# Optimization experiments

Hardware: AMD Instinct MI355X
Metric: run time of the kernel (lower is better)

## Reference

```python
import jax, jax.numpy as jnp
import numpy as np

N_NODES = 50000
N_EDGES = 800000
IN_CH = 128
OUT_CH = 32
HID = 2 * OUT_CH  # 64


def setup_inputs() -> dict:
    key = jax.random.key(0)
    ks = jax.random.split(key, 8)
    x = jax.random.normal(ks[0], (N_NODES, IN_CH), dtype=jnp.float32)
    edge_index = jax.random.randint(ks[1], (2, N_EDGES), 0, N_NODES, dtype=jnp.int32)
    s1 = 1.0 / np.sqrt(IN_CH)
    s2 = 1.0 / np.sqrt(HID)
    W1 = jax.random.normal(ks[2], (IN_CH, HID), dtype=jnp.float32) * s1
    b1 = jnp.zeros((HID,), dtype=jnp.float32)
    W_mu = jax.random.normal(ks[3], (HID, OUT_CH), dtype=jnp.float32) * s2
    b_mu = jnp.zeros((OUT_CH,), dtype=jnp.float32)
    W_logstd = jax.random.normal(ks[4], (HID, OUT_CH), dtype=jnp.float32) * s2
    b_logstd = jnp.zeros((OUT_CH,), dtype=jnp.float32)
    return {"x": x, "edge_index": edge_index, "W1": W1, "b1": b1,
            "W_mu": W_mu, "b_mu": b_mu, "W_logstd": W_logstd, "b_logstd": b_logstd}


def _gcn_norm(edge_index, n, dtype):
    # PyG GCNConv: add self-loops, symmetric normalization D^-1/2 A D^-1/2
    loops = jnp.arange(n, dtype=edge_index.dtype)
    src = jnp.concatenate([edge_index[0], loops])
    dst = jnp.concatenate([edge_index[1], loops])
    deg = jax.ops.segment_sum(jnp.ones_like(dst, dtype=dtype), dst, num_segments=n)
    deg_inv_sqrt = jnp.where(deg > 0, jax.lax.rsqrt(deg), 0.0)
    norm = deg_inv_sqrt[src] * deg_inv_sqrt[dst]  # [E+N]
    return src, dst, norm


def _gcn_conv(x, W, b, src, dst, norm, n):
    h = x @ W                        # transform first (in >= out)
    msg = h[src] * norm[:, None]     # gather + scale, [E+N, out]
    out = jax.ops.segment_sum(msg, dst, num_segments=n)
    return out + b


def reference(x, edge_index, W1, b1, W_mu, b_mu, W_logstd, b_logstd):
    n = x.shape[0]
    src, dst, norm = _gcn_norm(edge_index, n, x.dtype)
    h = jax.nn.relu(_gcn_conv(x, W1, b1, src, dst, norm, n))
    mu = _gcn_conv(h, W_mu, b_mu, src, dst, norm, n)
    logstd = _gcn_conv(h, W_logstd, b_logstd, src, dst, norm, n)
    return mu, logstd
```

## Files before the change

### kernel.cpp

```cpp
#include <hip/hip_runtime.h>
#include <hip/hip_fp16.h>

#define N_NODES 50000
#define N_EDGES 800000
#define IN_CH 128
#define HID 64
#define OUT_CH 32
#define CAP 64
#define ZROW N_NODES
#define CURS 16

union H4 { uint2 u; __half2 h[2]; };

__global__ __launch_bounds__(256) void k_scatter(const int* __restrict__ ei,
                                                 int* cur, unsigned short* __restrict__ pk,
                                                 unsigned* zA, unsigned* zB) {
    if (blockIdx.x == 0 && threadIdx.x < 32) { zA[threadIdx.x] = 0u; zB[threadIdx.x] = 0u; }
    int g = blockIdx.x * 256 + threadIdx.x;
    if (g >= N_EDGES / 2) return;
    int2 ss = ((const int2*)ei)[g];
    int2 dd = ((const int2*)(ei + N_EDGES))[g];
    int p0 = (dd.x << 6) + atomicAdd(&cur[dd.x << 4], 1);
    pk[p0] = (unsigned short)ss.x;
    int p1 = (dd.y << 6) + atomicAdd(&cur[dd.y << 4], 1);
    pk[p1] = (unsigned short)ss.y;
}

__global__ __launch_bounds__(256) void k_mm1(const float* __restrict__ x,
                                             const float* __restrict__ W1,
                                             const int* __restrict__ cur,
                                             __half* __restrict__ t1) {
    __shared__ float4 ws[64 * 16];
    __shared__ float  xsT[64 * 64];
    int t = threadIdx.x;
    int n0 = blockIdx.x * 64;
    int lane = t & 63, wv_ = t >> 6;
    int ni = lane >> 2;
    int cq = ((lane & 3) << 2) + wv_;
    const float4* W4 = (const float4*)W1;
    const float4* x4 = (const float4*)x;
    float4 acc0 = {0,0,0,0}, acc1 = acc0, acc2 = acc0, acc3 = acc0;
#pragma unroll
    for (int kt = 0; kt < 2; ++kt) {
        __syncthreads();
#pragma unroll
        for (int i = 0; i < 4; ++i) {
            int L = i * 256 + t;
            ws[L] = W4[kt * 1024 + L];
            int n = L >> 4, q = L & 15;
            int ng = n0 + n; if (ng >= N_NODES) ng = N_NODES - 1;
            float4 v = x4[ng * 32 + kt * 16 + q];
            int fb = q * 256 + (((n >> 2) ^ q) << 2) + (n & 3);
            xsT[fb]       = v.x;
            xsT[fb + 64]  = v.y;
            xsT[fb + 128] = v.z;
            xsT[fb + 192] = v.w;
        }
        __syncthreads();
        const float4* xsT4 = (const float4*)xsT;
#pragma unroll 8
        for (int k = 0; k < 64; ++k) {
            float4 xv = xsT4[k * 16 + (ni ^ (k >> 2))];
            float4 wvv = ws[k * 16 + cq];
            acc0.x += xv.x * wvv.x; acc0.y += xv.x * wvv.y; acc0.z += xv.x * wvv.z; acc0.w += xv.x * wvv.w;
            acc1.x += xv.y * wvv.x; acc1.y += xv.y * wvv.y; acc1.z += xv.y * wvv.z; acc1.w += xv.y * wvv.w;
            acc2.x += xv.z * wvv.x; acc2.y += xv.z * wvv.y; acc2.z += xv.z * wvv.z; acc2.w += xv.z * wvv.w;
            acc3.x += xv.w * wvv.x; acc3.y += xv.w * wvv.y; acc3.z += xv.w * wvv.z; acc3.w += xv.w * wvv.w;
        }
    }
    int nb = n0 + 4 * ni;
    if (nb < N_NODES) {
        float d0 = rsqrtf((float)cur[(nb + 0) << 4] + 1.0f);
        float d1 = rsqrtf((float)cur[(nb + 1) << 4] + 1.0f);
        float d2 = rsqrtf((float)cur[(nb + 2) << 4] + 1.0f);
        float d3 = rsqrtf((float)cur[(nb + 3) << 4] + 1.0f);
        uint2* o2 = (uint2*)t1;
        H4 v;
        v.h[0] = __floats2half2_rn(d0 * acc0.x, d0 * acc0.y);
        v.h[1] = __floats2half2_rn(d0 * acc0.z, d0 * acc0.w);
        o2[(nb + 0) * 16 + cq] = v.u;
        v.h[0] = __floats2half2_rn(d1 * acc1.x, d1 * acc1.y);
        v.h[1] = __floats2half2_rn(d1 * acc1.z, d1 * acc1.w);
        o2[(nb + 1) * 16 + cq] = v.u;
        v.h[0] = __floats2half2_rn(d2 * acc2.x, d2 * acc2.y);
        v.h[1] = __floats2half2_rn(d2 * acc2.z, d2 * acc2.w);
        o2[(nb + 2) * 16 + cq] = v.u;
        v.h[0] = __floats2half2_rn(d3 * acc3.x, d3 * acc3.y);
        v.h[1] = __floats2half2_rn(d3 * acc3.z, d3 * acc3.w);
        o2[(nb + 3) * 16 + cq] = v.u;
    }
}

__global__ __launch_bounds__(256) void k_agg(const unsigned short* __restrict__ pk,
                                             const int* __restrict__ cur,
                                             const __half* __restrict__ in,
                                             const float* __restrict__ bias,
                                             __half* __restrict__ out,
                                             int apply_relu) {
    int w = (blockIdx.x * 256 + threadIdx.x) >> 6;
    if (w >= N_NODES) return;
    int lane = threadIdx.x & 63;
    int eg = lane >> 3, cs = lane & 7;
    int cnt = __builtin_amdgcn_readfirstlane(cur[w << 4]);
    const uint4* __restrict__ inv = (const uint4*)in;
    float acc[8] = {0,0,0,0,0,0,0,0};
    if (eg * 8 < cnt) {
        uint4 p4 = ((const uint4*)pk)[w * 8 + eg];
        const unsigned short* us = (const unsigned short*)&p4;
#pragma unroll
        for (int i = 0; i < 8; ++i) {
            int s = (eg * 8 + i < cnt) ? (int)us[i] : ZROW;
            uint4 r = inv[s * 8 + cs];
            const __half2* h2 = (const __half2*)&r;
            float2 f;
            f = __half22float2(h2[0]); acc[0] += f.x; acc[1] += f.y;
            f = __half22float2(h2[1]); acc[2] += f.x; acc[3] += f.y;
            f = __half22float2(h2[2]); acc[4] += f.x; acc[5] += f.y;
            f = __half22float2(h2[3]); acc[6] += f.x; acc[7] += f.y;
        }
    }
#pragma unroll
    for (int m = 8; m <= 32; m <<= 1)
#pragma unroll
        for (int i = 0; i < 8; ++i) acc[i] += __shfl_xor(acc[i], m, 64);
    if (eg == 0) {
        uint4 sr = inv[w * 8 + cs];
        const __half2* sh = (const __half2*)&sr;
        float2 f;
        f = __half22float2(sh[0]); acc[0] += f.x; acc[1] += f.y;
        f = __half22float2(sh[1]); acc[2] += f.x; acc[3] += f.y;
        f = __half22float2(sh[2]); acc[4] += f.x; acc[5] += f.y;
        f = __half22float2(sh[3]); acc[6] += f.x; acc[7] += f.y;
        float dw = rsqrtf((float)cnt + 1.0f);
        if (apply_relu) {
            float4 b0 = ((const float4*)bias)[2 * cs];
            float4 b1v = ((const float4*)bias)[2 * cs + 1];
            acc[0] = dw * fmaxf(dw * acc[0] + b0.x, 0.f);
            acc[1] = dw * fmaxf(dw * acc[1] + b0.y, 0.f);
            acc[2] = dw * fmaxf(dw * acc[2] + b0.z, 0.f);
            acc[3] = dw * fmaxf(dw * acc[3] + b0.w, 0.f);
            acc[4] = dw * fmaxf(dw * acc[4] + b1v.x, 0.f);
            acc[5] = dw * fmaxf(dw * acc[5] + b1v.y, 0.f);
            acc[6] = dw * fmaxf(dw * acc[6] + b1v.z, 0.f);
            acc[7] = dw * fmaxf(dw * acc[7] + b1v.w, 0.f);
        } else {
#pragma unroll
            for (int i = 0; i < 8; ++i) acc[i] *= dw;
        }
        __half2 o[4];
        o[0] = __floats2half2_rn(acc[0], acc[1]);
        o[1] = __floats2half2_rn(acc[2], acc[3]);
        o[2] = __floats2half2_rn(acc[4], acc[5]);
        o[3] = __floats2half2_rn(acc[6], acc[7]);
        ((uint4*)out)[w * 8 + cs] = *(const uint4*)o;
    }
}

__global__ __launch_bounds__(256) void k_mm2(const __half* __restrict__ agg2,
                                             const float* __restrict__ Wmu,
                                             const float* __restrict__ bmu,
                                             const float* __restrict__ Wls,
                                             const float* __restrict__ bls,
                                             float* __restrict__ out) {
    __shared__ float4 ws[64 * 16];
    __shared__ float  xsT[64 * 64];
    int t = threadIdx.x;
    int n0 = blockIdx.x * 64;
    int lane = t & 63, wv_ = t >> 6;
    int ni = lane >> 2;
    int cq = ((lane & 3) << 2) + wv_;
    const float4* Wm4 = (const float4*)Wmu;
    const float4* Wl4 = (const float4*)Wls;
    const uint2*  x2  = (const uint2*)agg2;
#pragma unroll
    for (int i = 0; i < 4; ++i) {
        int L = i * 256 + t;
        int k = L >> 4, c = L & 15;
        ws[L] = (c < 8) ? Wm4[k * 8 + c] : Wl4[k * 8 + (c - 8)];
        int n = L >> 4, q = L & 15;
        int ng = n0 + n; if (ng >= N_NODES) ng = N_NODES - 1;
        H4 hv; hv.u = x2[ng * 16 + q];
        float2 f0 = __half22float2(hv.h[0]), f1 = __half22float2(hv.h[1]);
        int fb = q * 256 + (((n >> 2) ^ q) << 2) + (n & 3);
        xsT[fb]       = f0.x;
        xsT[fb + 64]  = f0.y;
        xsT[fb + 128] = f1.x;
        xsT[fb + 192] = f1.y;
    }
    float4 b = (cq < 8) ? ((const float4*)bmu)[cq] : ((const float4*)bls)[cq - 8];
    float4 acc0 = b, acc1 = b, acc2 = b, acc3 = b;
    __syncthreads();
    const float4* xsT4 = (const float4*)xsT;
#pragma unroll 8
    for (int k = 0; k < 64; ++k) {
        float4 xv = xsT4[k * 16 + (ni ^ (k >> 2))];
        float4 wvv = ws[k * 16 + cq];
        acc0.x += xv.x * wvv.x; acc0.y += xv.x * wvv.y; acc0.z += xv.x * wvv.z; acc0.w += xv.x * wvv.w;
        acc1.x += xv.y * wvv.x; acc1.y += xv.y * wvv.y; acc1.z += xv.y * wvv.z; acc1.w += xv.y * wvv.w;
        acc2.x += xv.z * wvv.x; acc2.y += xv.z * wvv.y; acc2.z += xv.z * wvv.z; acc2.w += xv.z * wvv.w;
        acc3.x += xv.w * wvv.x; acc3.y += xv.w * wvv.y; acc3.z += xv.w * wvv.z; acc3.w += xv.w * wvv.w;
    }
    int nb = n0 + 4 * ni;
    if (nb < N_NODES) {
        float4* o4 = (float4*)out;
        long base_off = (cq < 8) ? 0 : (long)N_NODES * 8;
        int cq8 = cq & 7;
        o4[base_off + (long)(nb + 0) * 8 + cq8] = acc0;
        o4[base_off + (long)(nb + 1) * 8 + cq8] = acc1;
        o4[base_off + (long)(nb + 2) * 8 + cq8] = acc2;
        o4[base_off + (long)(nb + 3) * 8 + cq8] = acc3;
    }
}

extern "C" void kernel_launch(void* const* d_in, const int* in_sizes, int n_in,
                              void* d_out, int out_size, void* d_ws, size_t ws_size,
                              hipStream_t stream) {
    const float* x   = (const float*)d_in[0];
    const int*   ei  = (const int*)  d_in[1];
    const float* W1  = (const float*)d_in[2];
    const float* b1  = (const float*)d_in[3];
    const float* Wmu = (const float*)d_in[4];
    const float* bmu = (const float*)d_in[5];
    const float* Wls = (const float*)d_in[6];
    const float* bls = (const float*)d_in[7];
    float* out = (float*)d_out;

    int*   cur  = (int*)d_ws;
    unsigned short* pk = (unsigned short*)((int*)d_ws + 800000);
    __half* bufA = (__half*)((int*)d_ws + 2400000);
    __half* bufB = (__half*)((int*)d_ws + 4000064);
    __half* bufC = (__half*)((int*)d_ws + 5600128);

    hipMemsetAsync(d_ws, 0, 3200000, stream);
    k_scatter <<<1563, 256, 0, stream>>>(ei, cur, pk,
                   (unsigned*)(bufA + (size_t)ZROW * HID),
                   (unsigned*)(bufB + (size_t)ZROW * HID));
    k_mm1     <<<782, 256, 0, stream>>>(x, W1, cur, bufA);
    k_agg     <<<12500, 256, 0, stream>>>(pk, cur, bufA, b1, bufB, 1);
    k_agg     <<<12500, 256, 0, stream>>>(pk, cur, bufB, nullptr, bufC, 0);
    k_mm2     <<<782, 256, 0, stream>>>(bufC, Wmu, bmu, Wls, bls, out);
}
```

Measured before the change: 206.5 us.

## Bucket CSR neighbor lists by source slice and partition scatter by destination

The scatter kernel now runs eight passes over the edge list, each handling only edges whose destination falls in one partition. Each destination's neighbors are bucketed into four source-range slices with separate compact counters, so the aggregation gathers neighbors in rough source order, which should improve cache locality for the feature reads. The padded, 16-stride counter array is replaced by dense per-slice counters, which shrinks the memset, and the zero-row padding trick is dropped. The cost is reading the destination array eight times, a loop over slices and rows in aggregation with more divergent lanes, and a fixed cap of 32 neighbors per slice that could overflow on skewed graphs.

Measured after the change: 265.5 us. 1.29x slower.

```diff
diff --git a/kernel.cpp b/kernel.cpp
--- a/kernel.cpp
+++ b/kernel.cpp
@@ -6,24 +6,35 @@
 #define IN_CH 128
 #define HID 64
 #define OUT_CH 32
-#define CAP 64
-#define ZROW N_NODES
-#define CURS 16
+#define NSLICE 4
+#define SLICE_SZ 12500
+#define SCAP 32
+#define PART_SZ 6250
+#define ROW_US 128
 
 union H4 { uint2 u; __half2 h[2]; };
 
 __global__ __launch_bounds__(256) void k_scatter(const int* __restrict__ ei,
-                                                 int* cur, unsigned short* __restrict__ pk,
-                                                 unsigned* zA, unsigned* zB) {
-    if (blockIdx.x == 0 && threadIdx.x < 32) { zA[threadIdx.x] = 0u; zB[threadIdx.x] = 0u; }
-    int g = blockIdx.x * 256 + threadIdx.x;
+                                                 int* cur,
+                                                 unsigned short* __restrict__ pk) {
+    int part = blockIdx.x & 7;
+    int g = (blockIdx.x >> 3) * 256 + threadIdx.x;
     if (g >= N_EDGES / 2) return;
+    int2 dd = ((const int2*)(ei + N_EDGES))[g];
+    bool a0 = (dd.x / PART_SZ) == part;
+    bool a1 = (dd.y / PART_SZ) == part;
+    if (!a0 && !a1) return;
     int2 ss = ((const int2*)ei)[g];
-    int2 dd = ((const int2*)(ei + N_EDGES))[g];
-    int p0 = (dd.x << 6) + atomicAdd(&cur[dd.x << 4], 1);
-    pk[p0] = (unsigned short)ss.x;
-    int p1 = (dd.y << 6) + atomicAdd(&cur[dd.y << 4], 1);
-    pk[p1] = (unsigned short)ss.y;
+    if (a0) {
+        int sl = ss.x / SLICE_SZ;
+        int pos = dd.x * ROW_US + sl * SCAP + atomicAdd(&cur[sl * N_NODES + dd.x], 1);
+        pk[pos] = (unsigned short)ss.x;
+    }
+    if (a1) {
+        int sl = ss.y / SLICE_SZ;
+        int pos = dd.y * ROW_US + sl * SCAP + atomicAdd(&cur[sl * N_NODES + dd.y], 1);
+        pk[pos] = (unsigned short)ss.y;
+    }
 }
 
 __global__ __launch_bounds__(256) void k_mm1(const float* __restrict__ x,
@@ -70,23 +81,26 @@
     }
     int nb = n0 + 4 * ni;
     if (nb < N_NODES) {
-        float d0 = rsqrtf((float)cur[(nb + 0) << 4] + 1.0f);
-        float d1 = rsqrtf((float)cur[(nb + 1) << 4] + 1.0f);
-        float d2 = rsqrtf((float)cur[(nb + 2) << 4] + 1.0f);
-        float d3 = rsqrtf((float)cur[(nb + 3) << 4] + 1.0f);
+        float dv[4];
+#pragma unroll
+        for (int j = 0; j < 4; ++j) {
+            int n = nb + j;
+            int c = cur[n] + cur[N_NODES + n] + cur[2 * N_NODES + n] + cur[3 * N_NODES + n];
+            dv[j] = rsqrtf((float)c + 1.0f);
+        }
         uint2* o2 = (uint2*)t1;
         H4 v;
-        v.h[0] = __floats2half2_rn(d0 * acc0.x, d0 * acc0.y);
-        v.h[1] = __floats2half2_rn(d0 * acc0.z, d0 * acc0.w);
+        v.h[0] = __floats2half2_rn(dv[0] * acc0.x, dv[0] * acc0.y);
+        v.h[1] = __floats2half2_rn(dv[0] * acc0.z, dv[0] * acc0.w);
         o2[(nb + 0) * 16 + cq] = v.u;
-        v.h[0] = __floats2half2_rn(d1 * acc1.x, d1 * acc1.y);
-        v.h[1] = __floats2half2_rn(d1 * acc1.z, d1 * acc1.w);
+        v.h[0] = __floats2half2_rn(dv[1] * acc1.x, dv[1] * acc1.y);
+        v.h[1] = __floats2half2_rn(dv[1] * acc1.z, dv[1] * acc1.w);
         o2[(nb + 1) * 16 + cq] = v.u;
-        v.h[0] = __floats2half2_rn(d2 * acc2.x, d2 * acc2.y);
-        v.h[1] = __floats2half2_rn(d2 * acc2.z, d2 * acc2.w);
+        v.h[0] = __floats2half2_rn(dv[2] * acc2.x, dv[2] * acc2.y);
+        v.h[1] = __floats2half2_rn(dv[2] * acc2.z, dv[2] * acc2.w);
         o2[(nb + 2) * 16 + cq] = v.u;
-        v.h[0] = __floats2half2_rn(d3 * acc3.x, d3 * acc3.y);
-        v.h[1] = __floats2half2_rn(d3 * acc3.z, d3 * acc3.w);
+        v.h[0] = __floats2half2_rn(dv[3] * acc3.x, dv[3] * acc3.y);
+        v.h[1] = __floats2half2_rn(dv[3] * acc3.z, dv[3] * acc3.w);
         o2[(nb + 3) * 16 + cq] = v.u;
     }
 }
@@ -101,22 +115,28 @@
     if (w >= N_NODES) return;
     int lane = threadIdx.x & 63;
     int eg = lane >> 3, cs = lane & 7;
-    int cnt = __builtin_amdgcn_readfirstlane(cur[w << 4]);
+    int c0 = __builtin_amdgcn_readfirstlane(cur[w]);
+    int c1 = __builtin_amdgcn_readfirstlane(cur[N_NODES + w]);
+    int c2 = __builtin_amdgcn_readfirstlane(cur[2 * N_NODES + w]);
+    int c3 = __builtin_amdgcn_readfirstlane(cur[3 * N_NODES + w]);
     const uint4* __restrict__ inv = (const uint4*)in;
     float acc[8] = {0,0,0,0,0,0,0,0};
-    if (eg * 8 < cnt) {
-        uint4 p4 = ((const uint4*)pk)[w * 8 + eg];
-        const unsigned short* us = (const unsigned short*)&p4;
-#pragma unroll
-        for (int i = 0; i < 8; ++i) {
-            int s = (eg * 8 + i < cnt) ? (int)us[i] : ZROW;
-            uint4 r = inv[s * 8 + cs];
-            const __half2* h2 = (const __half2*)&r;
-            float2 f;
-            f = __half22float2(h2[0]); acc[0] += f.x; acc[1] += f.y;
-            f = __half22float2(h2[1]); acc[2] += f.x; acc[3] += f.y;
-            f = __half22float2(h2[2]); acc[4] += f.x; acc[5] += f.y;
-            f = __half22float2(h2[3]); acc[6] += f.x; acc[7] += f.y;
+#pragma unroll
+    for (int s = 0; s < NSLICE; ++s) {
+        int c = (s == 0) ? c0 : (s == 1) ? c1 : (s == 2) ? c2 : c3;
+        for (int r = 0; r * 8 < c; ++r) {
+            uint4 p4 = ((const uint4*)pk)[w * 16 + s * 4 + r];
+            const unsigned short* us = (const unsigned short*)&p4;
+            if (r * 8 + eg < c) {
+                int src = (int)us[eg];
+                uint4 rr = inv[src * 8 + cs];
+                const __half2* h2 = (const __half2*)&rr;
+                float2 f;
+                f = __half22float2(h2[0]); acc[0] += f.x; acc[1] += f.y;
+                f = __half22float2(h2[1]); acc[2] += f.x; acc[3] += f.y;
+                f = __half22float2(h2[2]); acc[4] += f.x; acc[5] += f.y;
+                f = __half22float2(h2[3]); acc[6] += f.x; acc[7] += f.y;
+            }
         }
     }
 #pragma unroll
@@ -131,7 +151,7 @@
         f = __half22float2(sh[1]); acc[2] += f.x; acc[3] += f.y;
         f = __half22float2(sh[2]); acc[4] += f.x; acc[5] += f.y;
         f = __half22float2(sh[3]); acc[6] += f.x; acc[7] += f.y;
-        float dw = rsqrtf((float)cnt + 1.0f);
+        float dw = rsqrtf((float)(c0 + c1 + c2 + c3) + 1.0f);
         if (apply_relu) {
             float4 b0 = ((const float4*)bias)[2 * cs];
             float4 b1v = ((const float4*)bias)[2 * cs + 1];
@@ -226,15 +246,13 @@
     float* out = (float*)d_out;
 
     int*   cur  = (int*)d_ws;
-    unsigned short* pk = (unsigned short*)((int*)d_ws + 800000);
-    __half* bufA = (__half*)((int*)d_ws + 2400000);
-    __half* bufB = (__half*)((int*)d_ws + 4000064);
-    __half* bufC = (__half*)((int*)d_ws + 5600128);
-
-    hipMemsetAsync(d_ws, 0, 3200000, stream);
-    k_scatter <<<1563, 256, 0, stream>>>(ei, cur, pk,
-                   (unsigned*)(bufA + (size_t)ZROW * HID),
-                   (unsigned*)(bufB + (size_t)ZROW * HID));
+    unsigned short* pk = (unsigned short*)((int*)d_ws + 200000);
+    __half* bufA = (__half*)((int*)d_ws + 3400000);
+    __half* bufB = (__half*)((int*)d_ws + 5000000);
+    __half* bufC = (__half*)((int*)d_ws + 6600000);
+
+    hipMemsetAsync(d_ws, 0, 800000, stream);
+    k_scatter <<<1563 * 8, 256, 0, stream>>>(ei, cur, pk);
     k_mm1     <<<782, 256, 0, stream>>>(x, W1, cur, bufA);
     k_agg     <<<12500, 256, 0, stream>>>(pk, cur, bufA, b1, bufB, 1);
     k_agg     <<<12500, 256, 0, stream>>>(pk, cur, bufB, nullptr, bufC, 0);
```

## Split hidden features into two 32-channel halves and pack degree counters densely

Applied to the files above, without the earlier changes.

The 64-channel fp16 feature buffers are split into separate low and high 32-channel halves, and each aggregation pass runs twice, once per half. Each gathered row is then 64 bytes instead of 128, so the working set of each pass is halved, which should help L2/MALL hit rates on the random gathers. The per-node counters are also packed densely instead of padded to 16-int stride, which shrinks the memset and lets k_mm1 read four counts at once. In exchange the edge list is read twice as often, kernel launches double, and the dense counters add more atomic contention within a cache line.

Result: slower. 236.5 us (+14.5%).

```diff
diff --git a/kernel.cpp b/kernel.cpp
--- a/kernel.cpp
+++ b/kernel.cpp
@@ -8,28 +8,35 @@
 #define OUT_CH 32
 #define CAP 64
 #define ZROW N_NODES
-#define CURS 16
 
 union H4 { uint2 u; __half2 h[2]; };
 
 __global__ __launch_bounds__(256) void k_scatter(const int* __restrict__ ei,
                                                  int* cur, unsigned short* __restrict__ pk,
-                                                 unsigned* zA, unsigned* zB) {
-    if (blockIdx.x == 0 && threadIdx.x < 32) { zA[threadIdx.x] = 0u; zB[threadIdx.x] = 0u; }
+                                                 unsigned* zAlo, unsigned* zAhi,
+                                                 unsigned* zBlo, unsigned* zBhi) {
+    if (blockIdx.x == 0) {
+        int t = threadIdx.x;
+        if (t < 16) zAlo[t] = 0u;
+        else if (t < 32) zAhi[t - 16] = 0u;
+        else if (t < 48) zBlo[t - 32] = 0u;
+        else if (t < 64) zBhi[t - 48] = 0u;
+    }
     int g = blockIdx.x * 256 + threadIdx.x;
     if (g >= N_EDGES / 2) return;
     int2 ss = ((const int2*)ei)[g];
     int2 dd = ((const int2*)(ei + N_EDGES))[g];
-    int p0 = (dd.x << 6) + atomicAdd(&cur[dd.x << 4], 1);
+    int p0 = (dd.x << 6) + atomicAdd(&cur[dd.x], 1);
     pk[p0] = (unsigned short)ss.x;
-    int p1 = (dd.y << 6) + atomicAdd(&cur[dd.y << 4], 1);
+    int p1 = (dd.y << 6) + atomicAdd(&cur[dd.y], 1);
     pk[p1] = (unsigned short)ss.y;
 }
 
 __global__ __launch_bounds__(256) void k_mm1(const float* __restrict__ x,
                                              const float* __restrict__ W1,
                                              const int* __restrict__ cur,
-                                             __half* __restrict__ t1) {
+                                             __half* __restrict__ tlo,
+                                             __half* __restrict__ thi) {
     __shared__ float4 ws[64 * 16];
     __shared__ float  xsT[64 * 64];
     int t = threadIdx.x;
@@ -70,24 +77,27 @@
     }
     int nb = n0 + 4 * ni;
     if (nb < N_NODES) {
-        float d0 = rsqrtf((float)cur[(nb + 0) << 4] + 1.0f);
-        float d1 = rsqrtf((float)cur[(nb + 1) << 4] + 1.0f);
-        float d2 = rsqrtf((float)cur[(nb + 2) << 4] + 1.0f);
-        float d3 = rsqrtf((float)cur[(nb + 3) << 4] + 1.0f);
-        uint2* o2 = (uint2*)t1;
+        int4 c4 = *(const int4*)(cur + nb);
+        float d0 = rsqrtf((float)c4.x + 1.0f);
+        float d1 = rsqrtf((float)c4.y + 1.0f);
+        float d2 = rsqrtf((float)c4.z + 1.0f);
+        float d3 = rsqrtf((float)c4.w + 1.0f);
+        uint2* olo = (uint2*)tlo;
+        uint2* ohi = (uint2*)thi;
+        int cq8 = cq & 7;
         H4 v;
         v.h[0] = __floats2half2_rn(d0 * acc0.x, d0 * acc0.y);
         v.h[1] = __floats2half2_rn(d0 * acc0.z, d0 * acc0.w);
-        o2[(nb + 0) * 16 + cq] = v.u;
+        if (cq < 8) olo[(nb + 0) * 8 + cq8] = v.u; else ohi[(nb + 0) * 8 + cq8] = v.u;
         v.h[0] = __floats2half2_rn(d1 * acc1.x, d1 * acc1.y);
         v.h[1] = __floats2half2_rn(d1 * acc1.z, d1 * acc1.w);
-        o2[(nb + 1) * 16 + cq] = v.u;
+        if (cq < 8) olo[(nb + 1) * 8 + cq8] = v.u; else ohi[(nb + 1) * 8 + cq8] = v.u;
         v.h[0] = __floats2half2_rn(d2 * acc2.x, d2 * acc2.y);
         v.h[1] = __floats2half2_rn(d2 * acc2.z, d2 * acc2.w);
-        o2[(nb + 2) * 16 + cq] = v.u;
+        if (cq < 8) olo[(nb + 2) * 8 + cq8] = v.u; else ohi[(nb + 2) * 8 + cq8] = v.u;
         v.h[0] = __floats2half2_rn(d3 * acc3.x, d3 * acc3.y);
         v.h[1] = __floats2half2_rn(d3 * acc3.z, d3 * acc3.w);
-        o2[(nb + 3) * 16 + cq] = v.u;
+        if (cq < 8) olo[(nb + 3) * 8 + cq8] = v.u; else ohi[(nb + 3) * 8 + cq8] = v.u;
     }
 }
 
@@ -101,62 +111,52 @@
     if (w >= N_NODES) return;
     int lane = threadIdx.x & 63;
     int eg = lane >> 3, cs = lane & 7;
-    int cnt = __builtin_amdgcn_readfirstlane(cur[w << 4]);
-    const uint4* __restrict__ inv = (const uint4*)in;
-    float acc[8] = {0,0,0,0,0,0,0,0};
+    int cnt = __builtin_amdgcn_readfirstlane(cur[w]);
+    const uint2* __restrict__ inv = (const uint2*)in;
+    float acc[4] = {0,0,0,0};
     if (eg * 8 < cnt) {
         uint4 p4 = ((const uint4*)pk)[w * 8 + eg];
         const unsigned short* us = (const unsigned short*)&p4;
 #pragma unroll
         for (int i = 0; i < 8; ++i) {
             int s = (eg * 8 + i < cnt) ? (int)us[i] : ZROW;
-            uint4 r = inv[s * 8 + cs];
-            const __half2* h2 = (const __half2*)&r;
-            float2 f;
-            f = __half22float2(h2[0]); acc[0] += f.x; acc[1] += f.y;
-            f = __half22float2(h2[1]); acc[2] += f.x; acc[3] += f.y;
-            f = __half22float2(h2[2]); acc[4] += f.x; acc[5] += f.y;
-            f = __half22float2(h2[3]); acc[6] += f.x; acc[7] += f.y;
+            uint2 r = inv[s * 8 + cs];
+            __half2 h0 = *(__half2*)&r.x, h1 = *(__half2*)&r.y;
+            float2 f0 = __half22float2(h0), f1 = __half22float2(h1);
+            acc[0] += f0.x; acc[1] += f0.y; acc[2] += f1.x; acc[3] += f1.y;
         }
     }
 #pragma unroll
     for (int m = 8; m <= 32; m <<= 1)
 #pragma unroll
-        for (int i = 0; i < 8; ++i) acc[i] += __shfl_xor(acc[i], m, 64);
+        for (int i = 0; i < 4; ++i) acc[i] += __shfl_xor(acc[i], m, 64);
     if (eg == 0) {
-        uint4 sr = inv[w * 8 + cs];
-        const __half2* sh = (const __half2*)&sr;
-        float2 f;
-        f = __half22float2(sh[0]); acc[0] += f.x; acc[1] += f.y;
-        f = __half22float2(sh[1]); acc[2] += f.x; acc[3] += f.y;
-        f = __half22float2(sh[2]); acc[4] += f.x; acc[5] += f.y;
-        f = __half22float2(sh[3]); acc[6] += f.x; acc[7] += f.y;
+        uint2 sr = inv[w * 8 + cs];
+        __half2 s0 = *(__half2*)&sr.x, s1 = *(__half2*)&sr.y;
+        float2 f0 = __half22float2(s0), f1 = __half22float2(s1);
+        acc[0] += f0.x; acc[1] += f0.y; acc[2] += f1.x; acc[3] += f1.y;
         float dw = rsqrtf((float)cnt + 1.0f);
         if (apply_relu) {
-            float4 b0 = ((const float4*)bias)[2 * cs];
-            float4 b1v = ((const float4*)bias)[2 * cs + 1];
-            acc[0] = dw * fmaxf(dw * acc[0] + b0.x, 0.f);
-            acc[1] = dw * fmaxf(dw * acc[1] + b0.y, 0.f);
-            acc[2] = dw * fmaxf(dw * acc[2] + b0.z, 0.f);
-            acc[3] = dw * fmaxf(dw * acc[3] + b0.w, 0.f);
-            acc[4] = dw * fmaxf(dw * acc[4] + b1v.x, 0.f);
-            acc[5] = dw * fmaxf(dw * acc[5] + b1v.y, 0.f);
-            acc[6] = dw * fmaxf(dw * acc[6] + b1v.z, 0.f);
-            acc[7] = dw * fmaxf(dw * acc[7] + b1v.w, 0.f);
+            float4 b = ((const float4*)bias)[cs];
+            acc[0] = dw * fmaxf(dw * acc[0] + b.x, 0.f);
+            acc[1] = dw * fmaxf(dw * acc[1] + b.y, 0.f);
+            acc[2] = dw * fmaxf(dw * acc[2] + b.z, 0.f);
+            acc[3] = dw * fmaxf(dw * acc[3] + b.w, 0.f);
         } else {
 #pragma unroll
-            for (int i = 0; i < 8; ++i) acc[i] *= dw;
-        }
-        __half2 o[4];
-        o[0] = __floats2half2_rn(acc[0], acc[1]);
-        o[1] = __floats2half2_rn(acc[2], acc[3]);
-        o[2] = __floats2half2_rn(acc[4], acc[5]);
-        o[3] = __floats2half2_rn(acc[6], acc[7]);
-        ((uint4*)out)[w * 8 + cs] = *(const uint4*)o;
-    }
-}
-
-__global__ __launch_bounds__(256) void k_mm2(const __half* __restrict__ agg2,
+            for (int i = 0; i < 4; ++i) acc[i] *= dw;
+        }
+        __half2 o0 = __floats2half2_rn(acc[0], acc[1]);
+        __half2 o1 = __floats2half2_rn(acc[2], acc[3]);
+        uint2 ov;
+        ov.x = *(unsigned*)&o0;
+        ov.y = *(unsigned*)&o1;
+        ((uint2*)out)[w * 8 + cs] = ov;
+    }
+}
+
+__global__ __launch_bounds__(256) void k_mm2(const __half* __restrict__ clo,
+                                             const __half* __restrict__ chi,
                                              const float* __restrict__ Wmu,
                                              const float* __restrict__ bmu,
                                              const float* __restrict__ Wls,
@@ -171,7 +171,8 @@
     int cq = ((lane & 3) << 2) + wv_;
     const float4* Wm4 = (const float4*)Wmu;
     const float4* Wl4 = (const float4*)Wls;
-    const uint2*  x2  = (const uint2*)agg2;
+    const uint2*  xlo = (const uint2*)clo;
+    const uint2*  xhi = (const uint2*)chi;
 #pragma unroll
     for (int i = 0; i < 4; ++i) {
         int L = i * 256 + t;
@@ -179,7 +180,8 @@
         ws[L] = (c < 8) ? Wm4[k * 8 + c] : Wl4[k * 8 + (c - 8)];
         int n = L >> 4, q = L & 15;
         int ng = n0 + n; if (ng >= N_NODES) ng = N_NODES - 1;
-        H4 hv; hv.u = x2[ng * 16 + q];
+        H4 hv;
+        hv.u = (q < 8) ? xlo[ng * 8 + q] : xhi[ng * 8 + (q - 8)];
         float2 f0 = __half22float2(hv.h[0]), f1 = __half22float2(hv.h[1]);
         int fb = q * 256 + (((n >> 2) ^ q) << 2) + (n & 3);
         xsT[fb]       = f0.x;
@@ -226,17 +228,24 @@
     float* out = (float*)d_out;
 
     int*   cur  = (int*)d_ws;
-    unsigned short* pk = (unsigned short*)((int*)d_ws + 800000);
-    __half* bufA = (__half*)((int*)d_ws + 2400000);
-    __half* bufB = (__half*)((int*)d_ws + 4000064);
-    __half* bufC = (__half*)((int*)d_ws + 5600128);
-
-    hipMemsetAsync(d_ws, 0, 3200000, stream);
+    unsigned short* pk = (unsigned short*)((int*)d_ws + 50048);
+    __half* Alo = (__half*)((int*)d_ws + 1650048);
+    __half* Ahi = (__half*)((int*)d_ws + 2450112);
+    __half* Blo = (__half*)((int*)d_ws + 3250176);
+    __half* Bhi = (__half*)((int*)d_ws + 4050240);
+    __half* Clo = (__half*)((int*)d_ws + 4850304);
+    __half* Chi = (__half*)((int*)d_ws + 5650368);
+
+    hipMemsetAsync(d_ws, 0, 200000, stream);
     k_scatter <<<1563, 256, 0, stream>>>(ei, cur, pk,
-                   (unsigned*)(bufA + (size_t)ZROW * HID),
-                   (unsigned*)(bufB + (size_t)ZROW * HID));
-    k_mm1     <<<782, 256, 0, stream>>>(x, W1, cur, bufA);
-    k_agg     <<<12500, 256, 0, stream>>>(pk, cur, bufA, b1, bufB, 1);
-    k_agg     <<<12500, 256, 0, stream>>>(pk, cur, bufB, nullptr, bufC, 0);
-    k_mm2     <<<782, 256, 0, stream>>>(bufC, Wmu, bmu, Wls, bls, out);
-}
+                   (unsigned*)(Alo + (size_t)ZROW * 32),
+                   (unsigned*)(Ahi + (size_t)ZROW * 32),
+                   (unsigned*)(Blo + (size_t)ZROW * 32),
+                   (unsigned*)(Bhi + (size_t)ZROW * 32));
+    k_mm1 <<<782, 256, 0, stream>>>(x, W1, cur, Alo, Ahi);
+    k_agg <<<12500, 256, 0, stream>>>(pk, cur, Alo, b1,      Blo, 1);
+    k_agg <<<12500, 256, 0, stream>>>(pk, cur, Ahi, b1 + 32, Bhi, 1);
+    k_agg <<<12500, 256, 0, stream>>>(pk, cur, Blo, nullptr, Clo, 0);
+    k_agg <<<12500, 256, 0, stream>>>(pk, cur, Bhi, nullptr, Chi, 0);
+    k_mm2 <<<782, 256, 0, stream>>>(Clo, Chi, Wmu, bmu, Wls, bls, out);
+}
```
